# Performance work log

Measured on AMD Instinct MI355X. Metric: run time of the kernel, lower is better.

The kernel has to match this reference:

```python
import jax, jax.numpy as jnp
import numpy as np

TEMP = 0.5
NUM_QUERIES = 256
NUM_NEGATIVES = 256
STRONG_THRESHOLD = 0.97


def _l2norm(x):
    n = jnp.sqrt(jnp.sum(x * x, axis=-1, keepdims=True))
    return x / jnp.maximum(n, 1e-12)


def _mls(mu0, mu1, s0, s1, w0, w1):
    # mutual likelihood score, mean over feature dim
    mu0 = _l2norm(mu0)
    mu1 = _l2norm(mu1)
    up = (mu0 * w0 - mu1 * w1) ** 2
    down = s0 * w0 + s1 * w1
    return -0.5 * jnp.mean(up / down + jnp.log(down), axis=-1)


def setup_inputs() -> dict:
    key = jax.random.key(0)
    B, C, H, W, S = 4, 32, 256, 256, 8
    ks = jax.random.split(key, 6)
    weights = jax.random.uniform(ks[0], (B, C, H, W), jnp.float32, 0.1, 1.0)
    mu = jax.random.normal(ks[1], (B, C, H, W), jnp.float32)
    sigma = jax.random.uniform(ks[2], (B, C, H, W), jnp.float32, 0.1, 1.0)
    cls = jax.random.randint(ks[3], (B, H, W), 0, S)
    label = jax.nn.one_hot(cls, S, axis=1, dtype=jnp.float32)  # [B,S,H,W]
    mask = (jax.random.uniform(ks[4], (B, 1, H, W)) < 0.7).astype(jnp.float32)
    prob = jax.random.uniform(ks[5], (B, S, H, W), jnp.float32)
    return {"weights": weights, "mu": mu, "sigma": sigma, "label": label, "mask": mask, "prob": prob}


def _rank_table(m, N):
    # m: bool [S, N]. table[s, r] = pixel index with rank r within class s.
    S = m.shape[0]
    ranks = jnp.cumsum(m, axis=1) - 1
    idx = jnp.where(m, ranks, N)  # out-of-range entries are dropped
    tbl = jnp.zeros((S, N), jnp.int32)
    rows = jnp.broadcast_to(jnp.arange(S)[:, None], (S, N))
    vals = jnp.broadcast_to(jnp.arange(N, dtype=jnp.int32)[None, :], (S, N))
    return tbl.at[rows, idx].set(vals, mode="drop")


def _forward(weights, mu, sigma, label, mask, prob):
    B, C, H, W = mu.shape
    S = label.shape[1]
    N = B * H * W
    Q, NEG = NUM_QUERIES, NUM_NEGATIVES
    mu_f = jnp.transpose(mu, (0, 2, 3, 1)).reshape(N, C)
    sig_f = jnp.transpose(sigma, (0, 2, 3, 1)).reshape(N, C)
    w_f = jnp.transpose(weights, (0, 2, 3, 1)).reshape(N, C)
    valid = jnp.transpose(label * mask, (1, 0, 2, 3)).reshape(S, N)  # [S,N]
    prob_f = jnp.transpose(prob, (1, 0, 2, 3)).reshape(S, N)
    vmask = valid > 0
    hmask = vmask & (prob_f < STRONG_THRESHOLD)
    count = jnp.sum(vmask, axis=1)
    hcount = jnp.sum(hmask, axis=1)
    # prototypes: masked sums over valid pixels (no_grad in original)
    inv_sig_w = w_f / sig_f
    proto_sigma = 1.0 / (valid @ inv_sig_w)                    # [S,C]
    proto_mu = proto_sigma * (valid @ (inv_sig_w * mu_f))      # [S,C]
    proto_weight = 1.0 / (valid @ (1.0 / w_f))                 # [S,C]
    proto_mu, proto_sigma, proto_weight = map(jax.lax.stop_gradient, (proto_mu, proto_sigma, proto_weight))
    tbl_valid = _rank_table(vmask, N)
    tbl_hard = _rank_table(hmask, N)
    keys = jax.random.split(jax.random.key(42), S)

    def per_class(i, key):
        k1, k2, k3 = jax.random.split(key, 3)
        # anchor sampling from hard pixels of class i (differentiable gather)
        ra = jnp.minimum((jax.random.uniform(k1, (Q,)) * hcount[i]).astype(jnp.int32), jnp.maximum(hcount[i] - 1, 0))
        apix = tbl_hard[i, ra]
        a_mu, a_sig, a_w = mu_f[apix], sig_f[apix], w_f[apix]
        # negative class distribution from prototype similarity
        order = (i + 1 + jnp.arange(S - 1)) % S
        sim = _mls(proto_mu[i][None], proto_mu[order], proto_sigma[i][None], proto_sigma[order], proto_weight[i][None], proto_weight[order])
        sim = jnp.where(count[order] > 0, sim, -jnp.inf)
        cls_pick = jax.random.categorical(k2, sim / TEMP, shape=(Q, NEG))
        neg_cls = order[cls_pick]                              # [Q,NEG]
        cnt = count[neg_cls]
        rn = jnp.minimum((jax.random.uniform(k3, (Q, NEG)) * cnt).astype(jnp.int32), jnp.maximum(cnt - 1, 0))
        npix = tbl_valid[neg_cls, rn]                          # [Q,NEG]
        n_mu = jax.lax.stop_gradient(mu_f[npix])
        n_sig = jax.lax.stop_gradient(sig_f[npix])
        n_w = jax.lax.stop_gradient(w_f[npix])
        pos_mu = jnp.broadcast_to(proto_mu[i], (Q, 1, C))
        pos_sig = jnp.broadcast_to(proto_sigma[i], (Q, 1, C))
        pos_w = jnp.broadcast_to(proto_weight[i], (Q, 1, C))
        all_mu = jnp.concatenate([pos_mu, n_mu], axis=1)       # [Q,1+NEG,C]
        all_sig = jnp.concatenate([pos_sig, n_sig], axis=1)
        all_w = jnp.concatenate([pos_w, n_w], axis=1)
        logits = _mls(a_mu[:, None], all_mu, a_sig[:, None], all_sig, a_w[:, None], all_w) / TEMP
        ce = jnp.mean(jax.nn.logsumexp(logits, axis=1) - logits[:, 0])
        ok = (hcount[i] > 0) & (count[i] > 0)
        return jnp.where(ok, ce, 0.0)

    losses = jax.vmap(per_class)(jnp.arange(S), keys)
    valid_num = jnp.sum(count > 0)
    return jnp.sum(losses) / valid_num.astype(losses.dtype)


def reference(weights, mu, sigma, label, mask, prob):
    return _forward(weights, mu, sigma, label, mask, prob)
```

## Files before the change

kernel.cpp:

```cpp
#include <hip/hip_runtime.h>
#include <hip/hip_fp16.h>
#include <stdint.h>


#define NPIX  262144
#define NCLS  8
#define NQ    256
#define NNEG  256
#define NE    257
#define NBLK  1024

typedef unsigned short u16;
typedef unsigned int   u32;

struct TFKeys { u32 k1[8][2], k2[8][2], k3[8][2]; };

__host__ __device__ inline void tf2x32(u32 k0, u32 k1, u32 x0, u32 x1, u32& o0, u32& o1) {
  u32 ks2 = k0 ^ k1 ^ 0x1BD11BDAu;
  x0 += k0; x1 += k1;
#define TFR(R) { x0 += x1; x1 = (x1 << (R)) | (x1 >> (32 - (R))); x1 ^= x0; }
  TFR(13) TFR(15) TFR(26) TFR(6)
  x0 += k1;  x1 += ks2 + 1u;
  TFR(17) TFR(29) TFR(16) TFR(24)
  x0 += ks2; x1 += k0 + 2u;
  TFR(13) TFR(15) TFR(26) TFR(6)
  x0 += k0;  x1 += k1 + 3u;
  TFR(17) TFR(29) TFR(16) TFR(24)
  x0 += k1;  x1 += ks2 + 4u;
  TFR(13) TFR(15) TFR(26) TFR(6)
  x0 += ks2; x1 += k0 + 5u;
#undef TFR
  o0 = x0; o1 = x1;
}

__device__ inline float bfv(u16 v) { return __uint_as_float(((u32)v) << 16); }
__device__ inline float lo16(u32 v) { return __uint_as_float(v << 16); }
__device__ inline float hi16(u32 v) { return __uint_as_float(v & 0xFFFF0000u); }
__device__ inline float u01(u32 bits) { return __uint_as_float((bits >> 9) | 0x3F800000u) - 1.0f; }
__device__ inline u32 rbits(u32 k0, u32 k1, u32 idx) { u32 a, b; tf2x32(k0, k1, 0u, idx, a, b); return a ^ b; }
__device__ inline u32 packPQ(float p, float q) {
  return (u32)__half_as_ushort(__float2half(p)) | ((u32)__half_as_ushort(__float2half(q)) << 16);
}
__device__ inline float2 unpackPQ(u32 v) {
  return make_float2(__half2float(__ushort_as_half((u16)(v & 0xFFFFu))),
                     __half2float(__ushort_as_half((u16)(v >> 16))));
}

__global__ __launch_bounds__(256) void k_flags(const u16* __restrict__ lab, const u16* __restrict__ msk,
                                               const u16* __restrict__ prb, unsigned char* __restrict__ flags,
                                               int* __restrict__ blockCnt,
                                               float* __restrict__ protoAcc, float* __restrict__ ceAcc,
                                               int* __restrict__ diag) {
  __shared__ int cnt[16];
  int tid = threadIdx.x;
  if (blockIdx.x == 0) {
    for (int i = tid; i < 768; i += 256) protoAcc[i] = 0.f;
    if (tid < 8) ceAcc[tid] = 0.f;
    if (tid == 0) diag[0] = 0;
  }
  if (tid < 16) cnt[tid] = 0;
  __syncthreads();
  int n = blockIdx.x * 256 + tid;
  int b = n >> 16, hw = n & 65535;
  float m = bfv(msk[(b << 16) + hw]);
  int cls = 0; bool v = false;
  for (int s = 0; s < 8; s++) {
    float l = bfv(lab[((size_t)(b * 8 + s) << 16) + hw]);
    if (l * m > 0.f) { cls = s; v = true; }
  }
  bool h = false;
  if (v) { float p = bfv(prb[((size_t)(b * 8 + cls) << 16) + hw]); h = p < 0.97f; }
  flags[n] = (unsigned char)(cls | (v ? 16 : 0) | (h ? 32 : 0));
  if (v) atomicAdd(&cnt[cls], 1);
  if (h) atomicAdd(&cnt[8 + cls], 1);
  __syncthreads();
  if (tid < 16) blockCnt[tid * NBLK + blockIdx.x] = cnt[tid];
}

__global__ __launch_bounds__(1024) void k_scan(const int* __restrict__ blockCnt, int* __restrict__ blockOff,
                                               int* __restrict__ counts) {
  int ctr = threadIdx.x >> 6, lane = threadIdx.x & 63;
  int run = 0;
  for (int ch = 0; ch < 16; ch++) {
    int bidx = ch * 64 + lane;
    int v = blockCnt[ctr * NBLK + bidx];
    int x = v;
    for (int d = 1; d < 64; d <<= 1) { int t = __shfl_up(x, d); if (lane >= d) x += t; }
    blockOff[ctr * NBLK + bidx] = run + x - v;
    run += __shfl(x, 63);
  }
  if (lane == 0) counts[ctr] = run;
}

__global__ __launch_bounds__(256) void k_place(const unsigned char* __restrict__ flags, const int* __restrict__ blockOff,
                                               int* __restrict__ tblV, int* __restrict__ tblH) {
  __shared__ int wcnt[4][16];
  int tid = threadIdx.x;
  int n = blockIdx.x * 256 + tid;
  int f = flags[n];
  int cls = f & 15; bool v = (f & 16) != 0, h = (f & 32) != 0;
  int wave = tid >> 6, lane = tid & 63;
  unsigned long long below = (1ull << lane) - 1ull;
  int rv = 0, rh = 0;
  for (int s = 0; s < 8; s++) {
    unsigned long long bv = __ballot(v && (cls == s));
    unsigned long long bh = __ballot(h && (cls == s));
    if (lane == 0) { wcnt[wave][s] = __popcll(bv); wcnt[wave][8 + s] = __popcll(bh); }
    if (cls == s) { rv = __popcll(bv & below); rh = __popcll(bh & below); }
  }
  __syncthreads();
  int preV = 0, preH = 0;
  for (int w2 = 0; w2 < wave; w2++) { preV += wcnt[w2][cls]; preH += wcnt[w2][8 + cls]; }
  if (v) tblV[(size_t)cls * NPIX + blockOff[cls * NBLK + blockIdx.x] + preV + rv] = n;
  if (h) tblH[(size_t)cls * NPIX + blockOff[(8 + cls) * NBLK + blockIdx.x] + preH + rh] = n;
}

__global__ __launch_bounds__(256) void k_pq(const u16* __restrict__ mu, const u16* __restrict__ wgt,
                                            const u16* __restrict__ sig, u32* __restrict__ PQ) {
  __shared__ u32 tile[256 * 33];
  int t = threadIdx.x;
  int n0 = blockIdx.x * 512;
  int b = n0 >> 16;
  int hwt = (n0 & 65535) + 2 * t;
  size_t cb = ((size_t)(b * 32)) << 16;
  u32 m2[32];
  float ss0 = 0.f, ss1 = 0.f;
  #pragma unroll
  for (int c = 0; c < 32; c++) {
    m2[c] = *(const u32*)(mu + cb + ((size_t)c << 16) + hwt);
    float a = lo16(m2[c]), d = hi16(m2[c]);
    ss0 += a * a; ss1 += d * d;
  }
  float rn0 = 1.0f / fmaxf(sqrtf(ss0), 1e-12f);
  float rn1 = 1.0f / fmaxf(sqrtf(ss1), 1e-12f);
  u32 pk0[32], pk1[32];
  #pragma unroll
  for (int c = 0; c < 32; c++) {
    u32 w2 = *(const u32*)(wgt + cb + ((size_t)c << 16) + hwt);
    u32 s2 = *(const u32*)(sig + cb + ((size_t)c << 16) + hwt);
    float p0 = lo16(m2[c]) * rn0 * lo16(w2);
    float p1 = hi16(m2[c]) * rn1 * hi16(w2);
    float q0 = lo16(s2) * lo16(w2);
    float q1 = hi16(s2) * hi16(w2);
    pk0[c] = packPQ(p0, q0);
    pk1[c] = packPQ(p1, q1);
  }
  #pragma unroll
  for (int ch = 0; ch < 2; ch++) {
    if ((t >> 7) == ch) {
      int l = t & 127;
      #pragma unroll
      for (int c = 0; c < 32; c++) {
        tile[(2 * l + 0) * 33 + c] = pk0[c];
        tile[(2 * l + 1) * 33 + c] = pk1[c];
      }
    }
    __syncthreads();
    uint4* dst = (uint4*)(PQ + (size_t)(n0 + ch * 256) * 32);
    for (int k = t; k < 2048; k += 256) {
      int p = k >> 3, c4 = (k & 7) * 4;
      dst[k] = make_uint4(tile[p * 33 + c4], tile[p * 33 + c4 + 1],
                          tile[p * 33 + c4 + 2], tile[p * 33 + c4 + 3]);
    }
    __syncthreads();
  }
}

__global__ __launch_bounds__(256) void k_proto(const u16* __restrict__ mu, const u16* __restrict__ wgt,
                                               const u16* __restrict__ sig, const int* __restrict__ tblV,
                                               const int* __restrict__ counts, float* __restrict__ protoAcc) {
  int ch = blockIdx.x & 7;
  int sc = blockIdx.x >> 3;
  int c  = sc & 31;
  int s  = sc >> 5;
  int cnt = counts[s];
  const int* row = tblV + (size_t)s * NPIX;
  float a0 = 0.f, a1 = 0.f, a2 = 0.f;
  int r = ch * 256 + threadIdx.x;
  for (; r + 6144 < cnt; r += 8192) {
    int p0 = row[r], p1 = row[r + 2048], p2 = row[r + 4096], p3 = row[r + 6144];
    size_t A0 = (((size_t)((p0 >> 16) * 32 + c)) << 16) + (p0 & 65535);
    size_t A1 = (((size_t)((p1 >> 16) * 32 + c)) << 16) + (p1 & 65535);
    size_t A2 = (((size_t)((p2 >> 16) * 32 + c)) << 16) + (p2 & 65535);
    size_t A3 = (((size_t)((p3 >> 16) * 32 + c)) << 16) + (p3 & 65535);
    float m0 = bfv(mu[A0]), w0 = bfv(wgt[A0]), s0 = bfv(sig[A0]);
    float m1 = bfv(mu[A1]), w1 = bfv(wgt[A1]), s1 = bfv(sig[A1]);
    float m2_ = bfv(mu[A2]), w2 = bfv(wgt[A2]), s2 = bfv(sig[A2]);
    float m3 = bfv(mu[A3]), w3 = bfv(wgt[A3]), s3 = bfv(sig[A3]);
    float i0 = w0 / s0, i1 = w1 / s1, i2 = w2 / s2, i3 = w3 / s3;
    a0 += i0; a1 += i0 * m0; a2 += 1.0f / w0;
    a0 += i1; a1 += i1 * m1; a2 += 1.0f / w1;
    a0 += i2; a1 += i2 * m2_; a2 += 1.0f / w2;
    a0 += i3; a1 += i3 * m3; a2 += 1.0f / w3;
  }
  for (; r < cnt; r += 2048) {
    int pix = row[r];
    size_t a = (((size_t)((pix >> 16) * 32 + c)) << 16) + (pix & 65535);
    float mv = bfv(mu[a]), wv = bfv(wgt[a]), sv = bfv(sig[a]);
    float isw = wv / sv;
    a0 += isw; a1 += isw * mv; a2 += 1.0f / wv;
  }
  #pragma unroll
  for (int d = 1; d < 64; d <<= 1) {
    a0 += __shfl_xor(a0, d);
    a1 += __shfl_xor(a1, d);
    a2 += __shfl_xor(a2, d);
  }
  if ((threadIdx.x & 63) == 0) {
    atomicAdd(&protoAcc[sc * 3 + 0], a0);
    atomicAdd(&protoAcc[sc * 3 + 1], a1);
    atomicAdd(&protoAcc[sc * 3 + 2], a2);
  }
}

__global__ void k_protoFinal(const float* __restrict__ protoAcc, const int* __restrict__ counts,
                             u32* __restrict__ protoPQ, float* __restrict__ simL,
                             int* __restrict__ diag) {
  __shared__ float sP[256], sQ[256];
  __shared__ int alive;
  int tid = threadIdx.x;
  if (tid == 0) alive = 0;
  float a0 = protoAcc[tid * 3 + 0], a1 = protoAcc[tid * 3 + 1], a2 = protoAcc[tid * 3 + 2];
  bool have = counts[tid >> 5] > 0;
  bool ok = (a0 > 0.f) && (a2 > 0.f);
  __syncthreads();
  if (have && !ok) atomicOr(diag, 2);
  if (have && ok) alive = 1;
  float psig = 1.0f / a0;
  float pmu  = psig * a1;
  float pw   = 1.0f / a2;
  float sq = (have && ok) ? pmu * pmu : 0.f;
  #pragma unroll
  for (int d = 1; d < 32; d <<= 1) sq += __shfl_xor(sq, d);
  float rn = 1.0f / fmaxf(sqrtf(sq), 1e-12f);
  float pP = (have && ok) ? pmu * rn * pw : 0.f;
  float pQ = (have && ok) ? psig * pw : 0.f;
  sP[tid] = pP; sQ[tid] = pQ;
  protoPQ[tid] = packPQ(pP, pQ);
  __syncthreads();
  if (tid == 0 && alive == 0) atomicOr(diag, 32);
  if (tid < 64) {
    int i = tid >> 3, j = tid & 7;
    if (j < 7) {
      int o = (i + 1 + j) & 7;
      float acc = 0.f;
      for (int c = 0; c < 32; c++) {
        float d = sP[i * 32 + c] - sP[o * 32 + c];
        float dn = sQ[i * 32 + c] + sQ[o * 32 + c];
        acc += d * d / dn + logf(dn);
      }
      float sim = -0.5f * (acc * (1.0f / 32.0f));
      simL[i * 8 + j] = (counts[o] > 0) ? (sim * 2.0f) : -INFINITY;
    }
  }
}

__global__ __launch_bounds__(256) void k_pick(TFKeys K, const float* __restrict__ simL,
                                              const int* __restrict__ counts, const int* __restrict__ tblV,
                                              const int* __restrict__ tblH,
                                              int* __restrict__ npix, int* __restrict__ apix) {
  int bid = blockIdx.x;
  if (bid >= 2048) {
    int i = bid - 2048, q = threadIdx.x;
    u32 bits = rbits(K.k1[i][0], K.k1[i][1], (u32)q);
    float u = u01(bits);
    int hc = counts[8 + i];
    int ra = (int)(u * (float)hc);
    int cap = hc - 1; if (cap < 0) cap = 0;
    if (ra > cap) ra = cap; if (ra < 0) ra = 0;
    int p = tblH[(size_t)i * NPIX + ra];
    if (p < 0) p = 0; if (p > NPIX - 1) p = NPIX - 1;
    apix[i * NQ + q] = p;
    return;
  }
  int t = bid * 256 + threadIdx.x;
  int i = t >> 16;
  u32 rem = (u32)(t & 65535);
  u32 k20 = K.k2[i][0], k21 = K.k2[i][1];
  float Lr[7];
  #pragma unroll
  for (int j = 0; j < 7; j++) Lr[j] = simL[i * 8 + j];
  float m = 0.f; int pick = 0;
  #pragma unroll
  for (int j = 0; j < 7; j++) {
    u32 bits = rbits(k20, k21, rem * 7u + (u32)j);
    float f = u01(bits);
    float u = fmaxf(f, 1.17549435e-38f);
    float g = -logf(-logf(u));
    float v = g + Lr[j];
    if (j == 0) { m = v; } else if (v > m) { m = v; pick = j; }
  }
  int nc = (i + 1 + pick) & 7;
  u32 bits3 = rbits(K.k3[i][0], K.k3[i][1], rem);
  float u3 = u01(bits3);
  int cnt = counts[nc];
  int rn = (int)(u3 * (float)cnt);
  int cap = cnt - 1; if (cap < 0) cap = 0;
  if (rn > cap) rn = cap; if (rn < 0) rn = 0;
  int p = tblV[(size_t)nc * NPIX + rn];
  if (p < 0) p = 0; if (p > NPIX - 1) p = NPIX - 1;
  npix[t] = p;
}

__global__ __launch_bounds__(256) void k_logits(const u32* __restrict__ PQ, const u32* __restrict__ protoPQ,
                                                const int* __restrict__ apix, const int* __restrict__ npix,
                                                float* __restrict__ lg) {
  int t = blockIdx.x * 256 + threadIdx.x;
  int i = t / (NQ * NE);
  int rem = t - i * (NQ * NE);
  int q = rem / NE;
  int e = rem - q * NE;
  int ap = apix[i * NQ + q];
  const uint4* A = (const uint4*)(PQ + (size_t)ap * 32);
  const uint4* B = (e == 0) ? (const uint4*)(protoPQ + i * 32)
                            : (const uint4*)(PQ + (size_t)npix[(i * NQ + q) * NNEG + (e - 1)] * 32);
  float acc = 0.f;
  #pragma unroll
  for (int k = 0; k < 8; k++) {
    uint4 ua = A[k], ub = B[k];
    float2 fa, fb; float d, dn;
    fa = unpackPQ(ua.x); fb = unpackPQ(ub.x); d = fa.x - fb.x; dn = fa.y + fb.y; acc += d * d / dn + __logf(dn);
    fa = unpackPQ(ua.y); fb = unpackPQ(ub.y); d = fa.x - fb.x; dn = fa.y + fb.y; acc += d * d / dn + __logf(dn);
    fa = unpackPQ(ua.z); fb = unpackPQ(ub.z); d = fa.x - fb.x; dn = fa.y + fb.y; acc += d * d / dn + __logf(dn);
    fa = unpackPQ(ua.w); fb = unpackPQ(ub.w); d = fa.x - fb.x; dn = fa.y + fb.y; acc += d * d / dn + __logf(dn);
  }
  lg[t] = -(acc * (1.0f / 32.0f));
}

__global__ __launch_bounds__(256) void k_lse(const float* __restrict__ lg, float* __restrict__ ceAcc,
                                             int* __restrict__ diag) {
  int gt = blockIdx.x * 256 + threadIdx.x;
  int wid = gt >> 6;
  int lane = threadIdx.x & 63;
  const float* L = lg + (size_t)wid * NE;
  float loc[5]; int cnt = 0;
  bool bad = false;
  float m = -INFINITY;
  for (int e = lane; e < NE; e += 64) { float v = L[e]; loc[cnt++] = v; bad |= !(v == v); if (v > m) m = v; }
  if (__ballot(bad) != 0ull && lane == 0) atomicOr(diag, 8);
  for (int d = 1; d < 64; d <<= 1) { float o = __shfl_xor(m, d); if (o > m) m = o; }
  float s = 0.f;
  for (int k = 0; k < cnt; k++) s += __expf(loc[k] - m);
  for (int d = 1; d < 64; d <<= 1) s += __shfl_xor(s, d);
  if (lane == 0) {
    int i = wid >> 8;
    float lse = m + __logf(s);
    atomicAdd(&ceAcc[i], lse - L[0]);
  }
}

__global__ void k_final(const float* __restrict__ ceAcc, const int* __restrict__ counts,
                        const int* __restrict__ diag, u32* __restrict__ out) {
  if (blockIdx.x == 0 && threadIdx.x == 0) {
    float loss = 0.f; int vn = 0;
    int db = diag[0];
    for (int i = 0; i < 8; i++) {
      if (counts[i] > 0) vn++;
      float ce = ceAcc[i];
      if (counts[i] > 0 && counts[8 + i] > 0) {
        if (!(ce == ce)) db |= 4;
        loss += ce * (1.0f / 256.0f);
      }
    }
    if (vn == 0) db |= 1;
    loss = loss / (float)vn;
    if (!(loss == loss) && db == 0) db = 16;
    if (db != 0) loss = 4096.0f * (float)(1 + db);
    u32 fb = __float_as_uint(loss);
    u32 bv = (fb + 0x7FFFu + ((fb >> 16) & 1u)) >> 16;
    out[0] = (fb & 0xFFFF0000u) | (bv & 0xFFFFu);
  }
}

extern "C" void kernel_launch(void* const* d_in, const int* in_sizes, int n_in,
                              void* d_out, int out_size, void* d_ws, size_t ws_size,
                              hipStream_t stream) {
  (void)in_sizes; (void)n_in; (void)out_size; (void)ws_size;
  const u16* wgt = (const u16*)d_in[0];
  const u16* mu  = (const u16*)d_in[1];
  const u16* sig = (const u16*)d_in[2];
  const u16* lab = (const u16*)d_in[3];
  const u16* msk = (const u16*)d_in[4];
  const u16* prb = (const u16*)d_in[5];

  char* wp = (char*)d_ws;
  auto take = [&](size_t bytes) -> void* { void* p = (void*)wp; wp += ((bytes + 255) & ~(size_t)255); return p; };
  u32*   PQ       = (u32*)  take((size_t)NPIX * 32 * 4);
  int*   tblV     = (int*)  take((size_t)NCLS * NPIX * 4);
  int*   tblH     = (int*)  take((size_t)NCLS * NPIX * 4);
  float* lg       = (float*)take((size_t)NCLS * NQ * NE * 4);
  int*   npix     = (int*)  take((size_t)NCLS * NQ * NNEG * 4);
  unsigned char* flags = (unsigned char*)take(NPIX);
  int*   blockCnt = (int*)  take(16 * NBLK * 4);
  int*   blockOff = (int*)  take(16 * NBLK * 4);
  float* protoAcc = (float*)take(768 * 4);
  u32*   protoPQ  = (u32*)  take(256 * 4);
  float* simL     = (float*)take(64 * 4);
  int*   counts   = (int*)  take(16 * 4);
  float* ceAcc    = (float*)take(8 * 4);
  int*   apix     = (int*)  take(NCLS * NQ * 4);
  int*   diag     = (int*)  take(4);

  TFKeys K;
  for (u32 i = 0; i < 8; i++) {
    u32 ki0, ki1;
    tf2x32(0u, 42u, 0u, i, ki0, ki1);
    tf2x32(ki0, ki1, 0u, 0u, K.k1[i][0], K.k1[i][1]);
    tf2x32(ki0, ki1, 0u, 1u, K.k2[i][0], K.k2[i][1]);
    tf2x32(ki0, ki1, 0u, 2u, K.k3[i][0], K.k3[i][1]);
  }

  k_flags<<<1024, 256, 0, stream>>>(lab, msk, prb, flags, blockCnt, protoAcc, ceAcc, diag);
  k_scan<<<1, 1024, 0, stream>>>(blockCnt, blockOff, counts);
  k_place<<<1024, 256, 0, stream>>>(flags, blockOff, tblV, tblH);
  k_pq<<<512, 256, 0, stream>>>(mu, wgt, sig, PQ);
  k_proto<<<2048, 256, 0, stream>>>(mu, wgt, sig, tblV, counts, protoAcc);
  k_protoFinal<<<1, 256, 0, stream>>>(protoAcc, counts, protoPQ, simL, diag);
  k_pick<<<2056, 256, 0, stream>>>(K, simL, counts, tblV, tblH, npix, apix);
  k_logits<<<2056, 256, 0, stream>>>(PQ, protoPQ, apix, npix, lg);
  k_lse<<<512, 256, 0, stream>>>(lg, ceAcc, diag);
  k_final<<<1, 64, 0, stream>>>(ceAcc, counts, diag, (u32*)d_out);
}
```

Before: 270.9 us.

## Fuse negative sampling, logits and logsumexp into one per-query kernel

The separate pick, logits and logsumexp kernels are merged into a single k_sample kernel, with one block per (class, query). Each block stages the anchor PQ row in shared memory, computes one negative logit per thread, and reduces the logsumexp across the block. This drops the npix and lg intermediate buffers, their global round trips and two launches. Separately, the k_proto block index mapping is reordered so that neighbouring blocks share a channel c across different classes s. The fused kernel adds two block-level barriers and serial work on thread 0 for the prototype logit.

```diff
diff --git a/kernel.cpp b/kernel.cpp
--- a/kernel.cpp
+++ b/kernel.cpp
@@ -138,12 +138,8 @@
   for (int c = 0; c < 32; c++) {
     u32 w2 = *(const u32*)(wgt + cb + ((size_t)c << 16) + hwt);
     u32 s2 = *(const u32*)(sig + cb + ((size_t)c << 16) + hwt);
-    float p0 = lo16(m2[c]) * rn0 * lo16(w2);
-    float p1 = hi16(m2[c]) * rn1 * hi16(w2);
-    float q0 = lo16(s2) * lo16(w2);
-    float q1 = hi16(s2) * hi16(w2);
-    pk0[c] = packPQ(p0, q0);
-    pk1[c] = packPQ(p1, q1);
+    pk0[c] = packPQ(lo16(m2[c]) * rn0 * lo16(w2), lo16(s2) * lo16(w2));
+    pk1[c] = packPQ(hi16(m2[c]) * rn1 * hi16(w2), hi16(s2) * hi16(w2));
   }
   #pragma unroll
   for (int ch = 0; ch < 2; ch++) {
@@ -170,9 +166,9 @@
                                                const u16* __restrict__ sig, const int* __restrict__ tblV,
                                                const int* __restrict__ counts, float* __restrict__ protoAcc) {
   int ch = blockIdx.x & 7;
-  int sc = blockIdx.x >> 3;
-  int c  = sc & 31;
-  int s  = sc >> 5;
+  int s  = (blockIdx.x >> 3) & 7;
+  int c  = blockIdx.x >> 6;
+  int sc = s * 32 + c;
   int cnt = counts[s];
   const int* row = tblV + (size_t)s * NPIX;
   float a0 = 0.f, a1 = 0.f, a2 = 0.f;
@@ -255,13 +251,18 @@
   }
 }
 
-__global__ __launch_bounds__(256) void k_pick(TFKeys K, const float* __restrict__ simL,
-                                              const int* __restrict__ counts, const int* __restrict__ tblV,
-                                              const int* __restrict__ tblH,
-                                              int* __restrict__ npix, int* __restrict__ apix) {
-  int bid = blockIdx.x;
-  if (bid >= 2048) {
-    int i = bid - 2048, q = threadIdx.x;
+__global__ __launch_bounds__(256) void k_sample(TFKeys K, const float* __restrict__ simL,
+                                                const int* __restrict__ counts,
+                                                const int* __restrict__ tblV, const int* __restrict__ tblH,
+                                                const u32* __restrict__ PQ, const u32* __restrict__ protoPQ,
+                                                float* __restrict__ ceAcc, int* __restrict__ diag) {
+  __shared__ __align__(16) u32 sA[32];
+  __shared__ float redM[4], redS[4];
+  __shared__ int sAp;
+  int blk = blockIdx.x;
+  int i = blk >> 8, q = blk & 255;
+  int t = threadIdx.x;
+  if (t == 0) {
     u32 bits = rbits(K.k1[i][0], K.k1[i][1], (u32)q);
     float u = u01(bits);
     int hc = counts[8 + i];
@@ -270,17 +271,16 @@
     if (ra > cap) ra = cap; if (ra < 0) ra = 0;
     int p = tblH[(size_t)i * NPIX + ra];
     if (p < 0) p = 0; if (p > NPIX - 1) p = NPIX - 1;
-    apix[i * NQ + q] = p;
-    return;
-  }
-  int t = bid * 256 + threadIdx.x;
-  int i = t >> 16;
-  u32 rem = (u32)(t & 65535);
+    sAp = p;
+  }
+  __syncthreads();
+  if (t < 32) sA[t] = PQ[(size_t)sAp * 32 + t];
+  u32 rem = (u32)(q * 256 + t);
   u32 k20 = K.k2[i][0], k21 = K.k2[i][1];
   float Lr[7];
   #pragma unroll
   for (int j = 0; j < 7; j++) Lr[j] = simL[i * 8 + j];
-  float m = 0.f; int pick = 0;
+  float mg = 0.f; int pick = 0;
   #pragma unroll
   for (int j = 0; j < 7; j++) {
     u32 bits = rbits(k20, k21, rem * 7u + (u32)j);
@@ -288,64 +288,63 @@
     float u = fmaxf(f, 1.17549435e-38f);
     float g = -logf(-logf(u));
     float v = g + Lr[j];
-    if (j == 0) { m = v; } else if (v > m) { m = v; pick = j; }
+    if (j == 0) { mg = v; } else if (v > mg) { mg = v; pick = j; }
   }
   int nc = (i + 1 + pick) & 7;
   u32 bits3 = rbits(K.k3[i][0], K.k3[i][1], rem);
   float u3 = u01(bits3);
-  int cnt = counts[nc];
-  int rn = (int)(u3 * (float)cnt);
-  int cap = cnt - 1; if (cap < 0) cap = 0;
-  if (rn > cap) rn = cap; if (rn < 0) rn = 0;
-  int p = tblV[(size_t)nc * NPIX + rn];
-  if (p < 0) p = 0; if (p > NPIX - 1) p = NPIX - 1;
-  npix[t] = p;
-}
-
-__global__ __launch_bounds__(256) void k_logits(const u32* __restrict__ PQ, const u32* __restrict__ protoPQ,
-                                                const int* __restrict__ apix, const int* __restrict__ npix,
-                                                float* __restrict__ lg) {
-  int t = blockIdx.x * 256 + threadIdx.x;
-  int i = t / (NQ * NE);
-  int rem = t - i * (NQ * NE);
-  int q = rem / NE;
-  int e = rem - q * NE;
-  int ap = apix[i * NQ + q];
-  const uint4* A = (const uint4*)(PQ + (size_t)ap * 32);
-  const uint4* B = (e == 0) ? (const uint4*)(protoPQ + i * 32)
-                            : (const uint4*)(PQ + (size_t)npix[(i * NQ + q) * NNEG + (e - 1)] * 32);
-  float acc = 0.f;
+  int cntv = counts[nc];
+  int rn = (int)(u3 * (float)cntv);
+  int cap2 = cntv - 1; if (cap2 < 0) cap2 = 0;
+  if (rn > cap2) rn = cap2; if (rn < 0) rn = 0;
+  int np = tblV[(size_t)nc * NPIX + rn];
+  if (np < 0) np = 0; if (np > NPIX - 1) np = NPIX - 1;
+  __syncthreads();
+  const uint4* A4 = (const uint4*)sA;
+  const uint4* B  = (const uint4*)(PQ + (size_t)np * 32);
+  float accN = 0.f;
   #pragma unroll
   for (int k = 0; k < 8; k++) {
-    uint4 ua = A[k], ub = B[k];
+    uint4 ua = A4[k], ub = B[k];
     float2 fa, fb; float d, dn;
-    fa = unpackPQ(ua.x); fb = unpackPQ(ub.x); d = fa.x - fb.x; dn = fa.y + fb.y; acc += d * d / dn + __logf(dn);
-    fa = unpackPQ(ua.y); fb = unpackPQ(ub.y); d = fa.x - fb.x; dn = fa.y + fb.y; acc += d * d / dn + __logf(dn);
-    fa = unpackPQ(ua.z); fb = unpackPQ(ub.z); d = fa.x - fb.x; dn = fa.y + fb.y; acc += d * d / dn + __logf(dn);
-    fa = unpackPQ(ua.w); fb = unpackPQ(ub.w); d = fa.x - fb.x; dn = fa.y + fb.y; acc += d * d / dn + __logf(dn);
-  }
-  lg[t] = -(acc * (1.0f / 32.0f));
-}
-
-__global__ __launch_bounds__(256) void k_lse(const float* __restrict__ lg, float* __restrict__ ceAcc,
-                                             int* __restrict__ diag) {
-  int gt = blockIdx.x * 256 + threadIdx.x;
-  int wid = gt >> 6;
-  int lane = threadIdx.x & 63;
-  const float* L = lg + (size_t)wid * NE;
-  float loc[5]; int cnt = 0;
-  bool bad = false;
-  float m = -INFINITY;
-  for (int e = lane; e < NE; e += 64) { float v = L[e]; loc[cnt++] = v; bad |= !(v == v); if (v > m) m = v; }
-  if (__ballot(bad) != 0ull && lane == 0) atomicOr(diag, 8);
-  for (int d = 1; d < 64; d <<= 1) { float o = __shfl_xor(m, d); if (o > m) m = o; }
-  float s = 0.f;
-  for (int k = 0; k < cnt; k++) s += __expf(loc[k] - m);
-  for (int d = 1; d < 64; d <<= 1) s += __shfl_xor(s, d);
-  if (lane == 0) {
-    int i = wid >> 8;
-    float lse = m + __logf(s);
-    atomicAdd(&ceAcc[i], lse - L[0]);
+    fa = unpackPQ(ua.x); fb = unpackPQ(ub.x); d = fa.x - fb.x; dn = fa.y + fb.y; accN += d * d / dn + __logf(dn);
+    fa = unpackPQ(ua.y); fb = unpackPQ(ub.y); d = fa.x - fb.x; dn = fa.y + fb.y; accN += d * d / dn + __logf(dn);
+    fa = unpackPQ(ua.z); fb = unpackPQ(ub.z); d = fa.x - fb.x; dn = fa.y + fb.y; accN += d * d / dn + __logf(dn);
+    fa = unpackPQ(ua.w); fb = unpackPQ(ub.w); d = fa.x - fb.x; dn = fa.y + fb.y; accN += d * d / dn + __logf(dn);
+  }
+  float lN = -(accN * (1.0f / 32.0f));
+  float l0 = 0.f;
+  if (t == 0) {
+    const uint4* B0 = (const uint4*)(protoPQ + i * 32);
+    float acc0 = 0.f;
+    #pragma unroll
+    for (int k = 0; k < 8; k++) {
+      uint4 ua = A4[k], ub = B0[k];
+      float2 fa, fb; float d, dn;
+      fa = unpackPQ(ua.x); fb = unpackPQ(ub.x); d = fa.x - fb.x; dn = fa.y + fb.y; acc0 += d * d / dn + __logf(dn);
+      fa = unpackPQ(ua.y); fb = unpackPQ(ub.y); d = fa.x - fb.x; dn = fa.y + fb.y; acc0 += d * d / dn + __logf(dn);
+      fa = unpackPQ(ua.z); fb = unpackPQ(ub.z); d = fa.x - fb.x; dn = fa.y + fb.y; acc0 += d * d / dn + __logf(dn);
+      fa = unpackPQ(ua.w); fb = unpackPQ(ub.w); d = fa.x - fb.x; dn = fa.y + fb.y; acc0 += d * d / dn + __logf(dn);
+    }
+    l0 = -(acc0 * (1.0f / 32.0f));
+  }
+  bool bad = !(lN == lN) || (t == 0 && !(l0 == l0));
+  if (__ballot(bad) != 0ull && (t & 63) == 0) atomicOr(diag, 8);
+  float lm = (t == 0) ? fmaxf(lN, l0) : lN;
+  #pragma unroll
+  for (int d = 1; d < 64; d <<= 1) lm = fmaxf(lm, __shfl_xor(lm, d));
+  if ((t & 63) == 0) redM[t >> 6] = lm;
+  __syncthreads();
+  float M = fmaxf(fmaxf(redM[0], redM[1]), fmaxf(redM[2], redM[3]));
+  float es = __expf(lN - M) + ((t == 0) ? __expf(l0 - M) : 0.f);
+  #pragma unroll
+  for (int d = 1; d < 64; d <<= 1) es += __shfl_xor(es, d);
+  if ((t & 63) == 0) redS[t >> 6] = es;
+  __syncthreads();
+  if (t == 0) {
+    float S = redS[0] + redS[1] + redS[2] + redS[3];
+    float ce = (M + __logf(S)) - l0;
+    atomicAdd(&ceAcc[i], ce);
   }
 }
 
@@ -388,8 +387,6 @@
   u32*   PQ       = (u32*)  take((size_t)NPIX * 32 * 4);
   int*   tblV     = (int*)  take((size_t)NCLS * NPIX * 4);
   int*   tblH     = (int*)  take((size_t)NCLS * NPIX * 4);
-  float* lg       = (float*)take((size_t)NCLS * NQ * NE * 4);
-  int*   npix     = (int*)  take((size_t)NCLS * NQ * NNEG * 4);
   unsigned char* flags = (unsigned char*)take(NPIX);
   int*   blockCnt = (int*)  take(16 * NBLK * 4);
   int*   blockOff = (int*)  take(16 * NBLK * 4);
@@ -398,7 +395,6 @@
   float* simL     = (float*)take(64 * 4);
   int*   counts   = (int*)  take(16 * 4);
   float* ceAcc    = (float*)take(8 * 4);
-  int*   apix     = (int*)  take(NCLS * NQ * 4);
   int*   diag     = (int*)  take(4);
 
   TFKeys K;
@@ -416,8 +412,6 @@
   k_pq<<<512, 256, 0, stream>>>(mu, wgt, sig, PQ);
   k_proto<<<2048, 256, 0, stream>>>(mu, wgt, sig, tblV, counts, protoAcc);
   k_protoFinal<<<1, 256, 0, stream>>>(protoAcc, counts, protoPQ, simL, diag);
-  k_pick<<<2056, 256, 0, stream>>>(K, simL, counts, tblV, tblH, npix, apix);
-  k_logits<<<2056, 256, 0, stream>>>(PQ, protoPQ, apix, npix, lg);
-  k_lse<<<512, 256, 0, stream>>>(lg, ceAcc, diag);
+  k_sample<<<2048, 256, 0, stream>>>(K, simL, counts, tblV, tblH, PQ, protoPQ, ceAcc, diag);
   k_final<<<1, 64, 0, stream>>>(ceAcc, counts, diag, (u32*)d_out);
 }
```

Result: faster. 232.5 us (-14.2%).
